# Kernel optimization log

Hardware: AMD Instinct MI355X
Metric: run time of the kernel (lower is better)

The kernel has to match this reference:

```python
import jax, jax.numpy as jnp
import numpy as np

H, F, E = 1024, 2816, 8   # hidden_size, intermediate_size, num_local_experts
B, S = 2, 2048
TOP_K = 2


def setup_inputs() -> dict:
    key = jax.random.key(0)
    ks = jax.random.split(key, 5)
    scale = 0.02
    return {
        "hidden_states": jax.random.normal(ks[0], (B, S, H), jnp.float32),
        "gate_w": jax.random.normal(ks[1], (E, H), jnp.float32) * scale,
        "w1": jax.random.normal(ks[2], (E, F, H), jnp.float32) * scale,
        "w3": jax.random.normal(ks[3], (E, F, H), jnp.float32) * scale,
        "w2": jax.random.normal(ks[4], (E, H, F), jnp.float32) * scale,
    }


def reference(hidden_states, gate_w, w1, w3, w2):
    b, s, h = hidden_states.shape
    e = gate_w.shape[0]
    T = b * s
    x = hidden_states.reshape(T, h)                      # [T, H]
    router_logits = x @ gate_w.T                         # [T, E]
    probs = jax.nn.softmax(router_logits, axis=-1)
    topw, sel = jax.lax.top_k(probs, TOP_K)              # [T, K]
    topw = topw / jnp.sum(topw, axis=-1, keepdims=True)  # renormalize over top-k
    # dense combine weights [T, E] (equivalent to the per-expert scatter/index_add)
    comb = jnp.zeros((T, e), x.dtype).at[jnp.arange(T)[:, None], sel].add(topw)
    hidden = jax.nn.silu(jnp.einsum('th,efh->etf', x, w1)) * jnp.einsum('th,efh->etf', x, w3)
    y = jnp.einsum('etf,ehf->eth', hidden, w2)           # [E, T, H]
    out = jnp.einsum('eth,te->th', y, comb)              # weighted scatter-combine
    return out.reshape(b, s, h), router_logits
```

## Files before the change

### kernel.cpp

```cpp
#include <hip/hip_runtime.h>
#include <hip/hip_bf16.h>
#include <stdint.h>

#define T_TOK 4096
#define H_DIM 1024
#define F_DIM 2816
#define E_NUM 8

typedef __attribute__((ext_vector_type(8))) __bf16 bf16x8;
typedef __attribute__((ext_vector_type(4))) float floatx4;
typedef __attribute__((address_space(3))) char lds_char;
typedef __attribute__((address_space(1))) const char glb_char;

__device__ __forceinline__ void gload16(const void* g, void* l) {
  __builtin_amdgcn_global_load_lds((glb_char*)g, (lds_char*)l, 16, 0, 0);
}

__device__ __forceinline__ unsigned pack2bf16(float a, float b) {
  unsigned ua = __builtin_bit_cast(unsigned, a);
  unsigned ub = __builtin_bit_cast(unsigned, b);
  ua += 0x7fffu + ((ua >> 16) & 1u);
  ub += 0x7fffu + ((ub >> 16) & 1u);
  return (ua >> 16) | (ub & 0xffff0000u);
}

__device__ __forceinline__ int swz(int row, int colb) {
  return (row * 128 + colb) ^ ((row & 7) << 4);
}

__global__ __launch_bounds__(256) void convert_kernel(
    const float* __restrict__ src, __hip_bfloat16* __restrict__ dst,
    int nchunk8) {
  int i = blockIdx.x * blockDim.x + threadIdx.x;
  const int stride = gridDim.x * blockDim.x;
  for (; i < nchunk8; i += stride) {
    const float4* s = (const float4*)(src + (size_t)i * 8);
    float4 a = s[0], b = s[1];
    uint4 p;
    p.x = pack2bf16(a.x, a.y); p.y = pack2bf16(a.z, a.w);
    p.z = pack2bf16(b.x, b.y); p.w = pack2bf16(b.z, b.w);
    *(uint4*)((char*)dst + (size_t)i * 16) = p;
  }
}

__global__ __launch_bounds__(256) void router_kernel(
    const float* __restrict__ x, const float* __restrict__ gate,
    float* __restrict__ logits_out, __hip_bfloat16* __restrict__ xb,
    int* __restrict__ counts, int* __restrict__ idx_list,
    float* __restrict__ wgt_list)
{
  const int wv = threadIdx.x >> 6;
  const int lane = threadIdx.x & 63;
  const int t = blockIdx.x * 4 + wv;

  const float4* xr = (const float4*)(x + (size_t)t * H_DIM);
  const float4* g4 = (const float4*)gate;

  float acc[E_NUM];
#pragma unroll
  for (int e = 0; e < E_NUM; ++e) acc[e] = 0.f;

  unsigned* xbo = (unsigned*)(xb + (size_t)t * H_DIM);
#pragma unroll
  for (int j = 0; j < 4; ++j) {
    int i = j * 64 + lane;
    float4 xv = xr[i];
    uint2 pk;
    pk.x = pack2bf16(xv.x, xv.y);
    pk.y = pack2bf16(xv.z, xv.w);
    *(uint2*)(xbo + i * 2) = pk;
#pragma unroll
    for (int e = 0; e < E_NUM; ++e) {
      float4 gv = g4[e * 256 + i];
      acc[e] += xv.x * gv.x + xv.y * gv.y + xv.z * gv.z + xv.w * gv.w;
    }
  }
#pragma unroll
  for (int off = 32; off > 0; off >>= 1) {
#pragma unroll
    for (int e = 0; e < E_NUM; ++e) acc[e] += __shfl_xor(acc[e], off, 64);
  }

  if (lane == 0) {
#pragma unroll
    for (int e = 0; e < E_NUM; ++e) logits_out[(size_t)t * E_NUM + e] = acc[e];
    int i0 = 0; float v0 = acc[0];
#pragma unroll
    for (int e = 1; e < E_NUM; ++e) if (acc[e] > v0) { v0 = acc[e]; i0 = e; }
    int i1 = -1; float v1 = -1e30f;
#pragma unroll
    for (int e = 0; e < E_NUM; ++e)
      if (e != i0 && acc[e] > v1) { v1 = acc[e]; i1 = e; }
    float p1 = __expf(v1 - v0);
    float w0 = 1.f / (1.f + p1);
    float w1 = p1 / (1.f + p1);
    int pos0 = atomicAdd(&counts[i0], 1);
    idx_list[i0 * T_TOK + pos0] = t;
    wgt_list[i0 * T_TOK + pos0] = w0;
    int pos1 = atomicAdd(&counts[i1], 1);
    idx_list[i1 * T_TOK + pos1] = t;
    wgt_list[i1 * T_TOK + pos1] = w1;
  }
}

__global__ void scan_kernel(const int* __restrict__ counts,
                            int* __restrict__ offsets) {
  if (threadIdx.x == 0) {
    int s = 0;
    for (int e = 0; e < E_NUM; ++e) { offsets[e] = s; s += counts[e]; }
  }
}

__global__ __launch_bounds__(256) void gemm1_kernel(
    const __hip_bfloat16* __restrict__ xb,
    const __hip_bfloat16* __restrict__ w1b,
    const __hip_bfloat16* __restrict__ w3b,
    const int* __restrict__ counts, const int* __restrict__ offsets,
    const int* __restrict__ idx_list, __hip_bfloat16* __restrict__ hidden)
{
  const int e = blockIdx.z;
  const int n_e = counts[e];
  const int tm = blockIdx.y;
  if (n_e == 0 || tm * 128 >= n_e) return;
  const int tn = blockIdx.x;
  const int f0 = tn * 128;
  const int off_e = offsets[e];

  __shared__ char sA[16384];
  __shared__ char sB1[16384];
  __shared__ char sB3[16384];

  const int tid = threadIdx.x;
  const int lane = tid & 63;
  const int wv = tid >> 6;
  const int wrow = (wv >> 1) * 64;
  const int wcol = (wv & 1) * 64;
  const int csw = ((lane & 7) ^ (lane >> 3)) * 16;
  const int rsub = lane >> 3;

  const char* xbp = (const char*)xb;
  size_t arow[4];
#pragma unroll
  for (int i = 0; i < 4; ++i) {
    int r = wv * 32 + i * 8 + rsub;
    int pos = tm * 128 + r;
    int p = pos < n_e ? pos : n_e - 1;
    arow[i] = (size_t)idx_list[e * T_TOK + p] * (H_DIM * 2);
  }
  const char* w1p = (const char*)w1b + ((size_t)e * F_DIM + f0) * (H_DIM * 2);
  const char* w3p = (const char*)w3b + ((size_t)e * F_DIM + f0) * (H_DIM * 2);

  floatx4 acc1[4][4], acc3[4][4];
#pragma unroll
  for (int m = 0; m < 4; ++m)
#pragma unroll
    for (int n = 0; n < 4; ++n)
#pragma unroll
      for (int r = 0; r < 4; ++r) { acc1[m][n][r] = 0.f; acc3[m][n][r] = 0.f; }

  for (int kt = 0; kt < H_DIM / 64; ++kt) {
    const int kb = kt * 128;
    __syncthreads();
#pragma unroll
    for (int i = 0; i < 4; ++i) {
      int r = wv * 32 + i * 8 + rsub;
      int ldsoff = wv * 4096 + i * 1024;
      gload16(xbp + arow[i] + kb + csw, sA + ldsoff);
      gload16(w1p + (size_t)r * (H_DIM * 2) + kb + csw, sB1 + ldsoff);
      gload16(w3p + (size_t)r * (H_DIM * 2) + kb + csw, sB3 + ldsoff);
    }
    asm volatile("s_waitcnt vmcnt(0)" ::: "memory");
    __syncthreads();
#pragma unroll
    for (int kk = 0; kk < 2; ++kk) {
      const int colb = kk * 64 + (lane >> 4) * 16;
      bf16x8 af[4], bf1[4], bf3[4];
#pragma unroll
      for (int m = 0; m < 4; ++m)
        af[m] = *(const bf16x8*)(sA + swz(wrow + m * 16 + (lane & 15), colb));
#pragma unroll
      for (int n = 0; n < 4; ++n) {
        bf1[n] = *(const bf16x8*)(sB1 + swz(wcol + n * 16 + (lane & 15), colb));
        bf3[n] = *(const bf16x8*)(sB3 + swz(wcol + n * 16 + (lane & 15), colb));
      }
#pragma unroll
      for (int m = 0; m < 4; ++m)
#pragma unroll
        for (int n = 0; n < 4; ++n) {
          acc1[m][n] = __builtin_amdgcn_mfma_f32_16x16x32_bf16(
              af[m], bf1[n], acc1[m][n], 0, 0, 0);
          acc3[m][n] = __builtin_amdgcn_mfma_f32_16x16x32_bf16(
              af[m], bf3[n], acc3[m][n], 0, 0, 0);
        }
    }
  }

#pragma unroll
  for (int m = 0; m < 4; ++m) {
#pragma unroll
    for (int r = 0; r < 4; ++r) {
      int rl = wrow + m * 16 + ((lane >> 4) << 2) + r;
      int pos = tm * 128 + rl;
      if (pos < n_e) {
        __hip_bfloat16* hrow = hidden + (size_t)(off_e + pos) * F_DIM + f0;
#pragma unroll
        for (int n = 0; n < 4; ++n) {
          float h1 = acc1[m][n][r];
          float h3 = acc3[m][n][r];
          float h = (h1 / (1.f + __expf(-h1))) * h3;
          hrow[wcol + n * 16 + (lane & 15)] = __float2bfloat16(h);
        }
      }
    }
  }
}

__global__ __launch_bounds__(256) void gemm2_kernel(
    const __hip_bfloat16* __restrict__ hidden,
    const __hip_bfloat16* __restrict__ w2b,
    const int* __restrict__ counts, const int* __restrict__ offsets,
    const int* __restrict__ idx_list, const float* __restrict__ wgt_list,
    float* __restrict__ out)
{
  const int e = blockIdx.z;
  const int n_e = counts[e];
  const int tm = blockIdx.y;
  if (n_e == 0 || tm * 128 >= n_e) return;
  const int tn = blockIdx.x;
  const int n0 = tn * 128;
  const int off_e = offsets[e];

  __shared__ short sA[128 * 64];
  __shared__ short sB[128 * 64];
  __shared__ int s_tok[128];
  __shared__ float s_wgt[128];

  const int tid = threadIdx.x;
  if (tid < 128) {
    int pos = tm * 128 + tid;
    if (pos < n_e) {
      s_tok[tid] = idx_list[e * T_TOK + pos];
      s_wgt[tid] = wgt_list[e * T_TOK + pos];
    } else {
      s_tok[tid] = -1;
      s_wgt[tid] = 0.f;
    }
  }
  const int lane = tid & 63;
  const int wv = tid >> 6;
  const int wrow = (wv >> 1) * 64;
  const int wcol = (wv & 1) * 64;
  const int cc = tid & 7;
  const int rbase = tid >> 3;

  floatx4 acc[4][4];
#pragma unroll
  for (int m = 0; m < 4; ++m)
#pragma unroll
    for (int n = 0; n < 4; ++n)
#pragma unroll
      for (int r = 0; r < 4; ++r) acc[m][n][r] = 0.f;

  const __hip_bfloat16* w2e = w2b + ((size_t)e * H_DIM + n0) * F_DIM;

  for (int kt = 0; kt < F_DIM / 64; ++kt) {
    const int k0 = kt * 64;
    __syncthreads();
#pragma unroll
    for (int i = 0; i < 4; ++i) {
      int r = rbase + 32 * i;
      int pos = tm * 128 + r;
      int pr = pos < n_e ? pos : n_e - 1;
      uint4 av = *(const uint4*)(hidden + (size_t)(off_e + pr) * F_DIM +
                                 k0 + cc * 8);
      *(uint4*)((char*)sA + swz(r, cc * 16)) = av;
      uint4 bv = *(const uint4*)(w2e + (size_t)r * F_DIM + k0 + cc * 8);
      *(uint4*)((char*)sB + swz(r, cc * 16)) = bv;
    }
    __syncthreads();
#pragma unroll
    for (int kk = 0; kk < 2; ++kk) {
      const int colb = kk * 64 + (lane >> 4) * 16;
      bf16x8 af[4], bf[4];
#pragma unroll
      for (int m = 0; m < 4; ++m)
        af[m] = *(const bf16x8*)((const char*)sA +
                                 swz(wrow + m * 16 + (lane & 15), colb));
#pragma unroll
      for (int n = 0; n < 4; ++n)
        bf[n] = *(const bf16x8*)((const char*)sB +
                                 swz(wcol + n * 16 + (lane & 15), colb));
#pragma unroll
      for (int m = 0; m < 4; ++m)
#pragma unroll
        for (int n = 0; n < 4; ++n)
          acc[m][n] = __builtin_amdgcn_mfma_f32_16x16x32_bf16(
              af[m], bf[n], acc[m][n], 0, 0, 0);
    }
  }

#pragma unroll
  for (int m = 0; m < 4; ++m) {
#pragma unroll
    for (int r = 0; r < 4; ++r) {
      int rl = wrow + m * 16 + ((lane >> 4) << 2) + r;
      int tok = s_tok[rl];
      if (tok >= 0) {
        float wgt = s_wgt[rl];
        float* orow = out + (size_t)tok * H_DIM + n0;
#pragma unroll
        for (int n = 0; n < 4; ++n)
          atomicAdd(&orow[wcol + n * 16 + (lane & 15)], wgt * acc[m][n][r]);
      }
    }
  }
}

__global__ __launch_bounds__(256) void gemm1_fb(
    const __hip_bfloat16* __restrict__ xb,
    const float* __restrict__ w1, const float* __restrict__ w3,
    const int* __restrict__ counts, const int* __restrict__ offsets,
    const int* __restrict__ idx_list, __hip_bfloat16* __restrict__ hidden)
{
  const int e = blockIdx.z;
  const int n_e = counts[e];
  const int tm = blockIdx.y;
  if (n_e == 0 || tm * 128 >= n_e) return;
  const int tn = blockIdx.x;
  const int f0 = tn * 128;
  const int off_e = offsets[e];

  __shared__ short sA[128 * 64];
  __shared__ short sB1[128 * 64];
  __shared__ short sB3[128 * 64];
  __shared__ int s_row[128];

  const int tid = threadIdx.x;
  if (tid < 128) {
    int pos = tm * 128 + tid;
    int p = pos < n_e ? pos : n_e - 1;
    s_row[tid] = idx_list[e * T_TOK + p];
  }
  const int lane = tid & 63;
  const int wv = tid >> 6;
  const int wrow = (wv >> 1) * 64;
  const int wcol = (wv & 1) * 64;
  const int cc = tid & 7;
  const int rbase = tid >> 3;

  floatx4 acc1[4][4], acc3[4][4];
#pragma unroll
  for (int m = 0; m < 4; ++m)
#pragma unroll
    for (int n = 0; n < 4; ++n)
#pragma unroll
      for (int r = 0; r < 4; ++r) { acc1[m][n][r] = 0.f; acc3[m][n][r] = 0.f; }

  const float* w1e = w1 + (size_t)e * F_DIM * H_DIM + (size_t)f0 * H_DIM;
  const float* w3e = w3 + (size_t)e * F_DIM * H_DIM + (size_t)f0 * H_DIM;

  for (int kt = 0; kt < H_DIM / 64; ++kt) {
    const int k0 = kt * 64;
    __syncthreads();
#pragma unroll
    for (int i = 0; i < 4; ++i) {
      int r = rbase + 32 * i;
      uint4 av = *(const uint4*)(xb + (size_t)s_row[r] * H_DIM + k0 + cc * 8);
      *(uint4*)((char*)sA + swz(r, cc * 16)) = av;
      const float4* p1 = (const float4*)(w1e + (size_t)r * H_DIM + k0 + cc * 8);
      float4 a1 = p1[0], b1 = p1[1];
      uint4 pb1;
      pb1.x = pack2bf16(a1.x, a1.y); pb1.y = pack2bf16(a1.z, a1.w);
      pb1.z = pack2bf16(b1.x, b1.y); pb1.w = pack2bf16(b1.z, b1.w);
      *(uint4*)((char*)sB1 + swz(r, cc * 16)) = pb1;
      const float4* p3 = (const float4*)(w3e + (size_t)r * H_DIM + k0 + cc * 8);
      float4 a3 = p3[0], b3 = p3[1];
      uint4 pb3;
      pb3.x = pack2bf16(a3.x, a3.y); pb3.y = pack2bf16(a3.z, a3.w);
      pb3.z = pack2bf16(b3.x, b3.y); pb3.w = pack2bf16(b3.z, b3.w);
      *(uint4*)((char*)sB3 + swz(r, cc * 16)) = pb3;
    }
    __syncthreads();
#pragma unroll
    for (int kk = 0; kk < 2; ++kk) {
      const int colb = kk * 64 + (lane >> 4) * 16;
      bf16x8 af[4], bf1[4], bf3[4];
#pragma unroll
      for (int m = 0; m < 4; ++m)
        af[m] = *(const bf16x8*)((const char*)sA +
                                 swz(wrow + m * 16 + (lane & 15), colb));
#pragma unroll
      for (int n = 0; n < 4; ++n) {
        bf1[n] = *(const bf16x8*)((const char*)sB1 +
                                  swz(wcol + n * 16 + (lane & 15), colb));
        bf3[n] = *(const bf16x8*)((const char*)sB3 +
                                  swz(wcol + n * 16 + (lane & 15), colb));
      }
#pragma unroll
      for (int m = 0; m < 4; ++m)
#pragma unroll
        for (int n = 0; n < 4; ++n) {
          acc1[m][n] = __builtin_amdgcn_mfma_f32_16x16x32_bf16(
              af[m], bf1[n], acc1[m][n], 0, 0, 0);
          acc3[m][n] = __builtin_amdgcn_mfma_f32_16x16x32_bf16(
              af[m], bf3[n], acc3[m][n], 0, 0, 0);
        }
    }
  }
#pragma unroll
  for (int m = 0; m < 4; ++m) {
#pragma unroll
    for (int r = 0; r < 4; ++r) {
      int rl = wrow + m * 16 + ((lane >> 4) << 2) + r;
      int pos = tm * 128 + rl;
      if (pos < n_e) {
        __hip_bfloat16* hrow = hidden + (size_t)(off_e + pos) * F_DIM + f0;
#pragma unroll
        for (int n = 0; n < 4; ++n) {
          float h1 = acc1[m][n][r];
          float h3 = acc3[m][n][r];
          float h = (h1 / (1.f + __expf(-h1))) * h3;
          hrow[wcol + n * 16 + (lane & 15)] = __float2bfloat16(h);
        }
      }
    }
  }
}

__global__ __launch_bounds__(256) void gemm2_fb(
    const __hip_bfloat16* __restrict__ hidden, const float* __restrict__ w2,
    const int* __restrict__ counts, const int* __restrict__ offsets,
    const int* __restrict__ idx_list, const float* __restrict__ wgt_list,
    float* __restrict__ out)
{
  const int e = blockIdx.z;
  const int n_e = counts[e];
  const int tm = blockIdx.y;
  if (n_e == 0 || tm * 128 >= n_e) return;
  const int tn = blockIdx.x;
  const int n0 = tn * 128;
  const int off_e = offsets[e];

  __shared__ short sA[128 * 64];
  __shared__ short sB[128 * 64];
  __shared__ int s_tok[128];
  __shared__ float s_wgt[128];

  const int tid = threadIdx.x;
  if (tid < 128) {
    int pos = tm * 128 + tid;
    if (pos < n_e) {
      s_tok[tid] = idx_list[e * T_TOK + pos];
      s_wgt[tid] = wgt_list[e * T_TOK + pos];
    } else {
      s_tok[tid] = -1;
      s_wgt[tid] = 0.f;
    }
  }
  const int lane = tid & 63;
  const int wv = tid >> 6;
  const int wrow = (wv >> 1) * 64;
  const int wcol = (wv & 1) * 64;
  const int cc = tid & 7;
  const int rbase = tid >> 3;

  floatx4 acc[4][4];
#pragma unroll
  for (int m = 0; m < 4; ++m)
#pragma unroll
    for (int n = 0; n < 4; ++n)
#pragma unroll
      for (int r = 0; r < 4; ++r) acc[m][n][r] = 0.f;

  const float* w2e = w2 + (size_t)e * H_DIM * F_DIM + (size_t)n0 * F_DIM;

  for (int kt = 0; kt < F_DIM / 64; ++kt) {
    const int k0 = kt * 64;
    __syncthreads();
#pragma unroll
    for (int i = 0; i < 4; ++i) {
      int r = rbase + 32 * i;
      int pos = tm * 128 + r;
      int pr = pos < n_e ? pos : n_e - 1;
      uint4 av = *(const uint4*)(hidden + (size_t)(off_e + pr) * F_DIM +
                                 k0 + cc * 8);
      *(uint4*)((char*)sA + swz(r, cc * 16)) = av;
      const float4* pb = (const float4*)(w2e + (size_t)r * F_DIM + k0 + cc * 8);
      float4 ba = pb[0], bb = pb[1];
      uint4 pk;
      pk.x = pack2bf16(ba.x, ba.y); pk.y = pack2bf16(ba.z, ba.w);
      pk.z = pack2bf16(bb.x, bb.y); pk.w = pack2bf16(bb.z, bb.w);
      *(uint4*)((char*)sB + swz(r, cc * 16)) = pk;
    }
    __syncthreads();
#pragma unroll
    for (int kk = 0; kk < 2; ++kk) {
      const int colb = kk * 64 + (lane >> 4) * 16;
      bf16x8 af[4], bf[4];
#pragma unroll
      for (int m = 0; m < 4; ++m)
        af[m] = *(const bf16x8*)((const char*)sA +
                                 swz(wrow + m * 16 + (lane & 15), colb));
#pragma unroll
      for (int n = 0; n < 4; ++n)
        bf[n] = *(const bf16x8*)((const char*)sB +
                                 swz(wcol + n * 16 + (lane & 15), colb));
#pragma unroll
      for (int m = 0; m < 4; ++m)
#pragma unroll
        for (int n = 0; n < 4; ++n)
          acc[m][n] = __builtin_amdgcn_mfma_f32_16x16x32_bf16(
              af[m], bf[n], acc[m][n], 0, 0, 0);
    }
  }
#pragma unroll
  for (int m = 0; m < 4; ++m) {
#pragma unroll
    for (int r = 0; r < 4; ++r) {
      int rl = wrow + m * 16 + ((lane >> 4) << 2) + r;
      int tok = s_tok[rl];
      if (tok >= 0) {
        float wgt = s_wgt[rl];
        float* orow = out + (size_t)tok * H_DIM + n0;
#pragma unroll
        for (int n = 0; n < 4; ++n)
          atomicAdd(&orow[wcol + n * 16 + (lane & 15)], wgt * acc[m][n][r]);
      }
    }
  }
}

extern "C" void kernel_launch(void* const* d_in, const int* in_sizes, int n_in,
                              void* d_out, int out_size, void* d_ws,
                              size_t ws_size, hipStream_t stream) {
  const float* x = (const float*)d_in[0];
  const float* gate = (const float*)d_in[1];
  const float* w1 = (const float*)d_in[2];
  const float* w3 = (const float*)d_in[3];
  const float* w2 = (const float*)d_in[4];

  float* out = (float*)d_out;
  float* logits = out + (size_t)T_TOK * H_DIM;

  char* ws = (char*)d_ws;
  const size_t WEB = (size_t)E_NUM * F_DIM * H_DIM * 2;
  const size_t o_idx = 256;
  const size_t o_wgt = o_idx + (size_t)E_NUM * T_TOK * 4;
  const size_t o_xb  = o_wgt + (size_t)E_NUM * T_TOK * 4;
  const size_t o_hid = o_xb + (size_t)T_TOK * H_DIM * 2;
  const size_t o_w1b = o_hid + (size_t)2 * T_TOK * F_DIM * 2;
  const size_t o_w3b = o_w1b + WEB;
  const size_t o_w2b = o_w3b + WEB;
  const size_t need  = o_w2b + WEB;

  int* counts = (int*)ws;
  int* offsets = counts + 8;
  int* idx_list = (int*)(ws + o_idx);
  float* wgt_list = (float*)(ws + o_wgt);
  __hip_bfloat16* xb = (__hip_bfloat16*)(ws + o_xb);
  __hip_bfloat16* hidden = (__hip_bfloat16*)(ws + o_hid);

  hipMemsetAsync(counts, 0, 64, stream);
  hipMemsetAsync(out, 0, (size_t)T_TOK * H_DIM * sizeof(float), stream);

  if (ws_size >= need) {
    __hip_bfloat16* w1b = (__hip_bfloat16*)(ws + o_w1b);
    __hip_bfloat16* w3b = (__hip_bfloat16*)(ws + o_w3b);
    __hip_bfloat16* w2b = (__hip_bfloat16*)(ws + o_w2b);

    const int NCH = E_NUM * F_DIM * H_DIM / 8;
    convert_kernel<<<2048, 256, 0, stream>>>(w1, w1b, NCH);
    convert_kernel<<<2048, 256, 0, stream>>>(w3, w3b, NCH);
    convert_kernel<<<2048, 256, 0, stream>>>(w2, w2b, NCH);
    router_kernel<<<T_TOK / 4, 256, 0, stream>>>(x, gate, logits, xb, counts,
                                                 idx_list, wgt_list);
    scan_kernel<<<1, 64, 0, stream>>>(counts, offsets);
    gemm1_kernel<<<dim3(F_DIM / 128, T_TOK / 128, E_NUM), 256, 0, stream>>>(
        xb, w1b, w3b, counts, offsets, idx_list, hidden);
    gemm2_kernel<<<dim3(H_DIM / 128, T_TOK / 128, E_NUM), 256, 0, stream>>>(
        hidden, w2b, counts, offsets, idx_list, wgt_list, out);
  } else {
    router_kernel<<<T_TOK / 4, 256, 0, stream>>>(x, gate, logits, xb, counts,
                                                 idx_list, wgt_list);
    scan_kernel<<<1, 64, 0, stream>>>(counts, offsets);
    gemm1_fb<<<dim3(F_DIM / 128, T_TOK / 128, E_NUM), 256, 0, stream>>>(
        xb, w1, w3, counts, offsets, idx_list, hidden);
    gemm2_fb<<<dim3(H_DIM / 128, T_TOK / 128, E_NUM), 256, 0, stream>>>(
        hidden, w2, counts, offsets, idx_list, wgt_list, out);
  }
}
```

Before: 517.4 us.

## Interleave w1/w3 weights, double-buffer GEMMs, replace atomic scatter with combine kernel

Weights w1 and w3 are converted into a single interleaved bf16 matrix so gemm1 loads one B tile and computes both projections with larger 256x256 tiles on 512 threads. Both GEMMs now double-buffer LDS stages with async global-to-LDS loads, overlapping the next tile's fetch with the current tile's MFMA work. gemm2 writes per-expert bf16 outputs into a reused workspace region, and a new combine kernel gathers each token's two expert rows and blends them with the routing weights. This replaces fp32 atomic adds and removes the output memset. In exchange it uses more LDS per block and rounds y to bf16 before combining.

After: 446.8 us. -13.6%, faster.

```diff
diff --git a/kernel.cpp b/kernel.cpp
--- a/kernel.cpp
+++ b/kernel.cpp
@@ -22,6 +22,11 @@
   ua += 0x7fffu + ((ua >> 16) & 1u);
   ub += 0x7fffu + ((ub >> 16) & 1u);
   return (ua >> 16) | (ub & 0xffff0000u);
+}
+
+__device__ __forceinline__ float b2f(unsigned short u) {
+  unsigned v = ((unsigned)u) << 16;
+  return __builtin_bit_cast(float, v);
 }
 
 __device__ __forceinline__ int swz(int row, int colb) {
@@ -43,11 +48,30 @@
   }
 }
 
+__global__ __launch_bounds__(256) void convert_w13(
+    const float* __restrict__ w1, const float* __restrict__ w3,
+    __hip_bfloat16* __restrict__ wB) {
+  const int e = blockIdx.y;
+  const int rho = blockIdx.x * 2 + (threadIdx.x >> 7);
+  const int hc = threadIdx.x & 127;
+  const int f = ((rho >> 5) << 4) + (rho & 15);
+  const float* src = ((rho >> 4) & 1 ? w3 : w1) +
+                     ((size_t)e * F_DIM + f) * H_DIM + hc * 8;
+  const float4* s = (const float4*)src;
+  float4 a = s[0], b = s[1];
+  uint4 p;
+  p.x = pack2bf16(a.x, a.y); p.y = pack2bf16(a.z, a.w);
+  p.z = pack2bf16(b.x, b.y); p.w = pack2bf16(b.z, b.w);
+  *(uint4*)((char*)wB + (((size_t)e * (2 * F_DIM) + rho) * H_DIM + hc * 8) * 2)
+      = p;
+}
+
 __global__ __launch_bounds__(256) void router_kernel(
     const float* __restrict__ x, const float* __restrict__ gate,
     float* __restrict__ logits_out, __hip_bfloat16* __restrict__ xb,
     int* __restrict__ counts, int* __restrict__ idx_list,
-    float* __restrict__ wgt_list)
+    float* __restrict__ wgt_list, int* __restrict__ meta0,
+    int* __restrict__ meta1, float* __restrict__ wcomb)
 {
   const int wv = threadIdx.x >> 6;
   const int lane = threadIdx.x & 63;
@@ -100,6 +124,9 @@
     int pos1 = atomicAdd(&counts[i1], 1);
     idx_list[i1 * T_TOK + pos1] = t;
     wgt_list[i1 * T_TOK + pos1] = w1;
+    meta0[t] = (i0 << 16) | pos0;
+    meta1[t] = (i1 << 16) | pos1;
+    wcomb[t] = w0;
   }
 }
 
@@ -111,116 +138,127 @@
   }
 }
 
-__global__ __launch_bounds__(256) void gemm1_kernel(
+__global__ __launch_bounds__(512, 2) void gemm1_kernel(
     const __hip_bfloat16* __restrict__ xb,
-    const __hip_bfloat16* __restrict__ w1b,
-    const __hip_bfloat16* __restrict__ w3b,
+    const __hip_bfloat16* __restrict__ wB,
     const int* __restrict__ counts, const int* __restrict__ offsets,
     const int* __restrict__ idx_list, __hip_bfloat16* __restrict__ hidden)
 {
   const int e = blockIdx.z;
   const int n_e = counts[e];
   const int tm = blockIdx.y;
-  if (n_e == 0 || tm * 128 >= n_e) return;
+  if (n_e == 0 || tm * 256 >= n_e) return;
   const int tn = blockIdx.x;
-  const int f0 = tn * 128;
   const int off_e = offsets[e];
 
-  __shared__ char sA[16384];
-  __shared__ char sB1[16384];
-  __shared__ char sB3[16384];
+  __shared__ char lds[131072];
+  char* sA = lds;
+  char* sB = lds + 65536;
 
   const int tid = threadIdx.x;
   const int lane = tid & 63;
   const int wv = tid >> 6;
-  const int wrow = (wv >> 1) * 64;
-  const int wcol = (wv & 1) * 64;
-  const int csw = ((lane & 7) ^ (lane >> 3)) * 16;
-  const int rsub = lane >> 3;
-
+  const int wrow = (wv >> 2) * 128;
+  const int wcol = (wv & 3) * 64;
+  const int csw = ((lane & 7) ^ (lane >> 3)) << 4;
+  const int wvb = wv * 1024;
+
+  size_t aoff[4];
+#pragma unroll
+  for (int i = 0; i < 4; ++i) {
+    int r = i * 64 + wv * 8 + (lane >> 3);
+    int pos = tm * 256 + r;
+    int p = pos < n_e ? pos : n_e - 1;
+    aoff[i] = (size_t)idx_list[e * T_TOK + p] * 2048;
+  }
   const char* xbp = (const char*)xb;
-  size_t arow[4];
-#pragma unroll
-  for (int i = 0; i < 4; ++i) {
-    int r = wv * 32 + i * 8 + rsub;
-    int pos = tm * 128 + r;
-    int p = pos < n_e ? pos : n_e - 1;
-    arow[i] = (size_t)idx_list[e * T_TOK + p] * (H_DIM * 2);
-  }
-  const char* w1p = (const char*)w1b + ((size_t)e * F_DIM + f0) * (H_DIM * 2);
-  const char* w3p = (const char*)w3b + ((size_t)e * F_DIM + f0) * (H_DIM * 2);
-
-  floatx4 acc1[4][4], acc3[4][4];
-#pragma unroll
-  for (int m = 0; m < 4; ++m)
+  const char* wBp =
+      (const char*)wB + ((size_t)e * (2 * F_DIM) + tn * 256) * 2048;
+  size_t boff[4];
+#pragma unroll
+  for (int i = 0; i < 4; ++i)
+    boff[i] = (size_t)(i * 64 + wv * 8 + (lane >> 3)) * 2048;
+
+  floatx4 acc[8][4];
+#pragma unroll
+  for (int m = 0; m < 8; ++m)
 #pragma unroll
     for (int n = 0; n < 4; ++n)
 #pragma unroll
-      for (int r = 0; r < 4; ++r) { acc1[m][n][r] = 0.f; acc3[m][n][r] = 0.f; }
-
+      for (int r = 0; r < 4; ++r) acc[m][n][r] = 0.f;
+
+#define STAGE1(set, kb)                                                \
+  do {                                                                 \
+    char* dA = sA + (set) * 32768 + wvb;                               \
+    char* dB = sB + (set) * 32768 + wvb;                               \
+    _Pragma("unroll")                                                  \
+    for (int i = 0; i < 4; ++i) {                                      \
+      gload16(xbp + aoff[i] + (kb) + csw, dA + i * 8192);              \
+      gload16(wBp + boff[i] + (kb) + csw, dB + i * 8192);              \
+    }                                                                  \
+  } while (0)
+
+  asm volatile("s_waitcnt vmcnt(0)" ::: "memory");
+  STAGE1(0, 0);
+
+  int cur = 0;
   for (int kt = 0; kt < H_DIM / 64; ++kt) {
-    const int kb = kt * 128;
-    __syncthreads();
-#pragma unroll
-    for (int i = 0; i < 4; ++i) {
-      int r = wv * 32 + i * 8 + rsub;
-      int ldsoff = wv * 4096 + i * 1024;
-      gload16(xbp + arow[i] + kb + csw, sA + ldsoff);
-      gload16(w1p + (size_t)r * (H_DIM * 2) + kb + csw, sB1 + ldsoff);
-      gload16(w3p + (size_t)r * (H_DIM * 2) + kb + csw, sB3 + ldsoff);
-    }
-    asm volatile("s_waitcnt vmcnt(0)" ::: "memory");
-    __syncthreads();
+    if (kt < H_DIM / 64 - 1) {
+      STAGE1(cur ^ 1, (kt + 1) * 128);
+      asm volatile("s_waitcnt vmcnt(8)" ::: "memory");
+    } else {
+      asm volatile("s_waitcnt vmcnt(0)" ::: "memory");
+    }
+    __syncthreads();
+    const char* rA = sA + cur * 32768;
+    const char* rB = sB + cur * 32768;
 #pragma unroll
     for (int kk = 0; kk < 2; ++kk) {
       const int colb = kk * 64 + (lane >> 4) * 16;
-      bf16x8 af[4], bf1[4], bf3[4];
-#pragma unroll
-      for (int m = 0; m < 4; ++m)
-        af[m] = *(const bf16x8*)(sA + swz(wrow + m * 16 + (lane & 15), colb));
-#pragma unroll
-      for (int n = 0; n < 4; ++n) {
-        bf1[n] = *(const bf16x8*)(sB1 + swz(wcol + n * 16 + (lane & 15), colb));
-        bf3[n] = *(const bf16x8*)(sB3 + swz(wcol + n * 16 + (lane & 15), colb));
-      }
-#pragma unroll
-      for (int m = 0; m < 4; ++m)
-#pragma unroll
-        for (int n = 0; n < 4; ++n) {
-          acc1[m][n] = __builtin_amdgcn_mfma_f32_16x16x32_bf16(
-              af[m], bf1[n], acc1[m][n], 0, 0, 0);
-          acc3[m][n] = __builtin_amdgcn_mfma_f32_16x16x32_bf16(
-              af[m], bf3[n], acc3[m][n], 0, 0, 0);
-        }
-    }
-  }
-
-#pragma unroll
-  for (int m = 0; m < 4; ++m) {
+      bf16x8 af[8], bx[4];
+#pragma unroll
+      for (int m = 0; m < 8; ++m)
+        af[m] = *(const bf16x8*)(rA + swz(wrow + m * 16 + (lane & 15), colb));
+#pragma unroll
+      for (int n = 0; n < 4; ++n)
+        bx[n] = *(const bf16x8*)(rB + swz(wcol + n * 16 + (lane & 15), colb));
+#pragma unroll
+      for (int m = 0; m < 8; ++m)
+#pragma unroll
+        for (int n = 0; n < 4; ++n)
+          acc[m][n] = __builtin_amdgcn_mfma_f32_16x16x32_bf16(
+              af[m], bx[n], acc[m][n], 0, 0, 0);
+    }
+    __syncthreads();
+    cur ^= 1;
+  }
+#undef STAGE1
+
+  const int fbase = (tn * 8 + (wcol >> 5)) * 16 + (lane & 15);
+#pragma unroll
+  for (int m = 0; m < 8; ++m) {
 #pragma unroll
     for (int r = 0; r < 4; ++r) {
-      int rl = wrow + m * 16 + ((lane >> 4) << 2) + r;
-      int pos = tm * 128 + rl;
+      int pos = tm * 256 + wrow + m * 16 + ((lane >> 4) << 2) + r;
       if (pos < n_e) {
-        __hip_bfloat16* hrow = hidden + (size_t)(off_e + pos) * F_DIM + f0;
-#pragma unroll
-        for (int n = 0; n < 4; ++n) {
-          float h1 = acc1[m][n][r];
-          float h3 = acc3[m][n][r];
+        __hip_bfloat16* hrow = hidden + (size_t)(off_e + pos) * F_DIM;
+#pragma unroll
+        for (int j = 0; j < 2; ++j) {
+          float h1 = acc[m][2 * j][r];
+          float h3 = acc[m][2 * j + 1][r];
           float h = (h1 / (1.f + __expf(-h1))) * h3;
-          hrow[wcol + n * 16 + (lane & 15)] = __float2bfloat16(h);
+          hrow[fbase + j * 16] = __float2bfloat16(h);
         }
       }
     }
   }
 }
 
-__global__ __launch_bounds__(256) void gemm2_kernel(
+__global__ __launch_bounds__(256, 2) void gemm2_kernel(
     const __hip_bfloat16* __restrict__ hidden,
     const __hip_bfloat16* __restrict__ w2b,
     const int* __restrict__ counts, const int* __restrict__ offsets,
-    const int* __restrict__ idx_list, const float* __restrict__ wgt_list,
-    float* __restrict__ out)
+    __hip_bfloat16* __restrict__ y)
 {
   const int e = blockIdx.z;
   const int n_e = counts[e];
@@ -230,28 +268,29 @@
   const int n0 = tn * 128;
   const int off_e = offsets[e];
 
-  __shared__ short sA[128 * 64];
-  __shared__ short sB[128 * 64];
-  __shared__ int s_tok[128];
-  __shared__ float s_wgt[128];
+  __shared__ char lds[65536];
+  char* sA = lds;
+  char* sB = lds + 32768;
 
   const int tid = threadIdx.x;
-  if (tid < 128) {
-    int pos = tm * 128 + tid;
-    if (pos < n_e) {
-      s_tok[tid] = idx_list[e * T_TOK + pos];
-      s_wgt[tid] = wgt_list[e * T_TOK + pos];
-    } else {
-      s_tok[tid] = -1;
-      s_wgt[tid] = 0.f;
-    }
-  }
   const int lane = tid & 63;
   const int wv = tid >> 6;
   const int wrow = (wv >> 1) * 64;
   const int wcol = (wv & 1) * 64;
-  const int cc = tid & 7;
-  const int rbase = tid >> 3;
+  const int csw = ((lane & 7) ^ (lane >> 3)) << 4;
+  const int wvb = wv * 1024;
+
+  size_t aoff[4], boff[4];
+#pragma unroll
+  for (int i = 0; i < 4; ++i) {
+    int r = i * 32 + wv * 8 + (lane >> 3);
+    int pos = tm * 128 + r;
+    int p = pos < n_e ? pos : n_e - 1;
+    aoff[i] = (size_t)(off_e + p) * (F_DIM * 2);
+    boff[i] = ((size_t)e * H_DIM + n0 + r) * (F_DIM * 2);
+  }
+  const char* hp = (const char*)hidden;
+  const char* w2p = (const char*)w2b;
 
   floatx4 acc[4][4];
 #pragma unroll
@@ -261,59 +300,88 @@
 #pragma unroll
       for (int r = 0; r < 4; ++r) acc[m][n][r] = 0.f;
 
-  const __hip_bfloat16* w2e = w2b + ((size_t)e * H_DIM + n0) * F_DIM;
-
+#define STAGE2(set, kb)                                                \
+  do {                                                                 \
+    char* dA = sA + (set) * 16384 + wvb;                               \
+    char* dB = sB + (set) * 16384 + wvb;                               \
+    _Pragma("unroll")                                                  \
+    for (int i = 0; i < 4; ++i) {                                      \
+      gload16(hp + aoff[i] + (kb) + csw, dA + i * 4096);               \
+      gload16(w2p + boff[i] + (kb) + csw, dB + i * 4096);              \
+    }                                                                  \
+  } while (0)
+
+  asm volatile("s_waitcnt vmcnt(0)" ::: "memory");
+  STAGE2(0, 0);
+
+  int cur = 0;
   for (int kt = 0; kt < F_DIM / 64; ++kt) {
-    const int k0 = kt * 64;
-    __syncthreads();
-#pragma unroll
-    for (int i = 0; i < 4; ++i) {
-      int r = rbase + 32 * i;
-      int pos = tm * 128 + r;
-      int pr = pos < n_e ? pos : n_e - 1;
-      uint4 av = *(const uint4*)(hidden + (size_t)(off_e + pr) * F_DIM +
-                                 k0 + cc * 8);
-      *(uint4*)((char*)sA + swz(r, cc * 16)) = av;
-      uint4 bv = *(const uint4*)(w2e + (size_t)r * F_DIM + k0 + cc * 8);
-      *(uint4*)((char*)sB + swz(r, cc * 16)) = bv;
-    }
-    __syncthreads();
+    if (kt < F_DIM / 64 - 1) {
+      STAGE2(cur ^ 1, (kt + 1) * 128);
+      asm volatile("s_waitcnt vmcnt(8)" ::: "memory");
+    } else {
+      asm volatile("s_waitcnt vmcnt(0)" ::: "memory");
+    }
+    __syncthreads();
+    const char* rA = sA + cur * 16384;
+    const char* rB = sB + cur * 16384;
 #pragma unroll
     for (int kk = 0; kk < 2; ++kk) {
       const int colb = kk * 64 + (lane >> 4) * 16;
-      bf16x8 af[4], bf[4];
+      bf16x8 af[4], bx[4];
 #pragma unroll
       for (int m = 0; m < 4; ++m)
-        af[m] = *(const bf16x8*)((const char*)sA +
-                                 swz(wrow + m * 16 + (lane & 15), colb));
+        af[m] = *(const bf16x8*)(rA + swz(wrow + m * 16 + (lane & 15), colb));
 #pragma unroll
       for (int n = 0; n < 4; ++n)
-        bf[n] = *(const bf16x8*)((const char*)sB +
-                                 swz(wcol + n * 16 + (lane & 15), colb));
+        bx[n] = *(const bf16x8*)(rB + swz(wcol + n * 16 + (lane & 15), colb));
 #pragma unroll
       for (int m = 0; m < 4; ++m)
 #pragma unroll
         for (int n = 0; n < 4; ++n)
           acc[m][n] = __builtin_amdgcn_mfma_f32_16x16x32_bf16(
-              af[m], bf[n], acc[m][n], 0, 0, 0);
-    }
-  }
+              af[m], bx[n], acc[m][n], 0, 0, 0);
+    }
+    __syncthreads();
+    cur ^= 1;
+  }
+#undef STAGE2
 
 #pragma unroll
   for (int m = 0; m < 4; ++m) {
 #pragma unroll
     for (int r = 0; r < 4; ++r) {
-      int rl = wrow + m * 16 + ((lane >> 4) << 2) + r;
-      int tok = s_tok[rl];
-      if (tok >= 0) {
-        float wgt = s_wgt[rl];
-        float* orow = out + (size_t)tok * H_DIM + n0;
+      int pos = tm * 128 + wrow + m * 16 + ((lane >> 4) << 2) + r;
+      if (pos < n_e) {
+        __hip_bfloat16* yrow = y + (size_t)(off_e + pos) * H_DIM + n0;
 #pragma unroll
         for (int n = 0; n < 4; ++n)
-          atomicAdd(&orow[wcol + n * 16 + (lane & 15)], wgt * acc[m][n][r]);
+          yrow[wcol + n * 16 + (lane & 15)] = __float2bfloat16(acc[m][n][r]);
       }
     }
   }
+}
+
+__global__ __launch_bounds__(256) void combine_kernel(
+    const __hip_bfloat16* __restrict__ y, const int* __restrict__ offsets,
+    const int* __restrict__ meta0, const int* __restrict__ meta1,
+    const float* __restrict__ wcomb, float* __restrict__ out)
+{
+  const int t = blockIdx.x;
+  const int m0 = meta0[t], m1 = meta1[t];
+  const float w0 = wcomb[t];
+  const float w1 = 1.f - w0;
+  const size_t s0 = (size_t)(offsets[m0 >> 16] + (m0 & 0xffff)) * H_DIM;
+  const size_t s1 = (size_t)(offsets[m1 >> 16] + (m1 & 0xffff)) * H_DIM;
+  const int c = threadIdx.x * 4;
+  ushort4 a = *(const ushort4*)(y + s0 + c);
+  ushort4 b = *(const ushort4*)(y + s1 + c);
+  float4 o;
+  o.x = w0 * b2f(a.x) + w1 * b2f(b.x);
+  o.y = w0 * b2f(a.y) + w1 * b2f(b.y);
+  o.z = w0 * b2f(a.z) + w1 * b2f(b.z);
+  o.w = w0 * b2f(a.w) + w1 * b2f(b.w);
+  *(float4*)(out + (size_t)t * H_DIM + c) = o;
 }
 
 __global__ __launch_bounds__(256) void gemm1_fb(
@@ -543,45 +611,50 @@
   float* logits = out + (size_t)T_TOK * H_DIM;
 
   char* ws = (char*)d_ws;
-  const size_t WEB = (size_t)E_NUM * F_DIM * H_DIM * 2;
   const size_t o_idx = 256;
   const size_t o_wgt = o_idx + (size_t)E_NUM * T_TOK * 4;
-  const size_t o_xb  = o_wgt + (size_t)E_NUM * T_TOK * 4;
+  const size_t o_m0  = o_wgt + (size_t)E_NUM * T_TOK * 4;
+  const size_t o_m1  = o_m0 + (size_t)T_TOK * 4;
+  const size_t o_wc  = o_m1 + (size_t)T_TOK * 4;
+  const size_t o_xb  = o_wc + (size_t)T_TOK * 4;
   const size_t o_hid = o_xb + (size_t)T_TOK * H_DIM * 2;
-  const size_t o_w1b = o_hid + (size_t)2 * T_TOK * F_DIM * 2;
-  const size_t o_w3b = o_w1b + WEB;
-  const size_t o_w2b = o_w3b + WEB;
-  const size_t need  = o_w2b + WEB;
+  const size_t o_wB  = o_hid + (size_t)2 * T_TOK * F_DIM * 2;
+  const size_t o_w2b = o_wB + (size_t)E_NUM * 2 * F_DIM * H_DIM * 2;
+  const size_t need  = o_w2b + (size_t)E_NUM * H_DIM * F_DIM * 2;
 
   int* counts = (int*)ws;
   int* offsets = counts + 8;
   int* idx_list = (int*)(ws + o_idx);
   float* wgt_list = (float*)(ws + o_wgt);
+  int* meta0 = (int*)(ws + o_m0);
+  int* meta1 = (int*)(ws + o_m1);
+  float* wcomb = (float*)(ws + o_wc);
   __hip_bfloat16* xb = (__hip_bfloat16*)(ws + o_xb);
   __hip_bfloat16* hidden = (__hip_bfloat16*)(ws + o_hid);
 
   hipMemsetAsync(counts, 0, 64, stream);
-  hipMemsetAsync(out, 0, (size_t)T_TOK * H_DIM * sizeof(float), stream);
 
   if (ws_size >= need) {
-    __hip_bfloat16* w1b = (__hip_bfloat16*)(ws + o_w1b);
-    __hip_bfloat16* w3b = (__hip_bfloat16*)(ws + o_w3b);
+    __hip_bfloat16* wB = (__hip_bfloat16*)(ws + o_wB);
     __hip_bfloat16* w2b = (__hip_bfloat16*)(ws + o_w2b);
-
-    const int NCH = E_NUM * F_DIM * H_DIM / 8;
-    convert_kernel<<<2048, 256, 0, stream>>>(w1, w1b, NCH);
-    convert_kernel<<<2048, 256, 0, stream>>>(w3, w3b, NCH);
-    convert_kernel<<<2048, 256, 0, stream>>>(w2, w2b, NCH);
-    router_kernel<<<T_TOK / 4, 256, 0, stream>>>(x, gate, logits, xb, counts,
-                                                 idx_list, wgt_list);
+    __hip_bfloat16* y = (__hip_bfloat16*)(ws + o_wB);
+
+    convert_w13<<<dim3(F_DIM, E_NUM), 256, 0, stream>>>(w1, w3, wB);
+    convert_kernel<<<2048, 256, 0, stream>>>(
+        w2, w2b, E_NUM * F_DIM * H_DIM / 8);
+    router_kernel<<<T_TOK / 4, 256, 0, stream>>>(
+        x, gate, logits, xb, counts, idx_list, wgt_list, meta0, meta1, wcomb);
     scan_kernel<<<1, 64, 0, stream>>>(counts, offsets);
-    gemm1_kernel<<<dim3(F_DIM / 128, T_TOK / 128, E_NUM), 256, 0, stream>>>(
-        xb, w1b, w3b, counts, offsets, idx_list, hidden);
+    gemm1_kernel<<<dim3(2 * F_DIM / 256, T_TOK / 256, E_NUM), 512, 0,
+                   stream>>>(xb, wB, counts, offsets, idx_list, hidden);
     gemm2_kernel<<<dim3(H_DIM / 128, T_TOK / 128, E_NUM), 256, 0, stream>>>(
-        hidden, w2b, counts, offsets, idx_list, wgt_list, out);
+        hidden, w2b, counts, offsets, y);
+    combine_kernel<<<T_TOK, 256, 0, stream>>>(y, offsets, meta0, meta1, wcomb,
+                                              out);
   } else {
-    router_kernel<<<T_TOK / 4, 256, 0, stream>>>(x, gate, logits, xb, counts,
-                                                 idx_list, wgt_list);
+    hipMemsetAsync(out, 0, (size_t)T_TOK * H_DIM * sizeof(float), stream);
+    router_kernel<<<T_TOK / 4, 256, 0, stream>>>(
+        x, gate, logits, xb, counts, idx_list, wgt_list, meta0, meta1, wcomb);
     scan_kernel<<<1, 64, 0, stream>>>(counts, offsets);
     gemm1_fb<<<dim3(F_DIM / 128, T_TOK / 128, E_NUM), 256, 0, stream>>>(
         xb, w1, w3, counts, offsets, idx_list, hidden);
```
